# Optimization experiments

Hardware: AMD Instinct MI355X
Metric: run time of the kernel (lower is better)

The kernel has to match this reference:

```python
import jax, jax.numpy as jnp
import numpy as np

NUM_HARMONICS = 64
TEMPERATURE = 1.0

def setup_inputs() -> dict:
    key = jax.random.key(0)
    k1, k2 = jax.random.split(key)
    phases_q = jax.random.normal(k1, (2, 8, 2048, NUM_HARMONICS), dtype=jnp.float32)
    phases_k = jax.random.normal(k2, (2, 8, 2048, NUM_HARMONICS), dtype=jnp.float32)
    return {"phases_q": phases_q, "phases_k": phases_k}

def reference(phases_q, phases_k):
    # mean_h cos(q_h - k_h) = (cos_q @ cos_k^T + sin_q @ sin_k^T) / H
    # (identity: cos(a-b) = cos a cos b + sin a sin b) -- avoids the
    # O(Sq*Sk*H) broadcast intermediate of the naive formulation.
    cq, sq = jnp.cos(phases_q), jnp.sin(phases_q)
    ck, sk = jnp.cos(phases_k), jnp.sin(phases_k)
    coherence = (jnp.einsum('bhqd,bhkd->bhqk', cq, ck) +
                 jnp.einsum('bhqd,bhkd->bhqk', sq, sk)) / NUM_HARMONICS
    return coherence / TEMPERATURE
```

## Files before the change

kernel.cpp:

```cpp
#include <hip/hip_runtime.h>
#include <hip/hip_bf16.h>

#define SEQ 2048
#define NH  64
#define KP  128
#define NBATCH 16
#define STLD 68
#define STSZ (16 * STLD)

typedef __attribute__((ext_vector_type(8))) short  short8;
typedef __attribute__((ext_vector_type(4))) float  floatx4;

static __device__ __forceinline__ unsigned short f2bf(float f) {
    union { float f; unsigned u; } x; x.f = f;
    return (unsigned short)((x.u + 0x7fffu + ((x.u >> 16) & 1u)) >> 16);
}

__global__ void sincos_pack_kernel(const float* __restrict__ pq,
                                   const float* __restrict__ pk,
                                   unsigned short* __restrict__ qpack,
                                   unsigned short* __restrict__ kpack) {
    int i = blockIdx.x * blockDim.x + threadIdx.x;
    const float* src = blockIdx.y ? pk : pq;
    unsigned short* dst = blockIdx.y ? kpack : qpack;
    float4 v = ((const float4*)src)[i];
    int base = i << 2;
    int row  = base >> 6;
    int h    = base & 63;
    float s0, c0, s1, c1, s2, c2, s3, c3;
    __sincosf(v.x, &s0, &c0);
    __sincosf(v.y, &s1, &c1);
    __sincosf(v.z, &s2, &c2);
    __sincosf(v.w, &s3, &c3);
    ushort4 cu; cu.x = f2bf(c0); cu.y = f2bf(c1); cu.z = f2bf(c2); cu.w = f2bf(c3);
    ushort4 su; su.x = f2bf(s0); su.y = f2bf(s1); su.z = f2bf(s2); su.w = f2bf(s3);
    unsigned short* p = dst + (size_t)row * KP + h;
    *(ushort4*)p        = cu;
    *(ushort4*)(p + NH) = su;
}

__global__ __launch_bounds__(256, 2)
void coherence_gemm_kernel(const unsigned short* __restrict__ Qp,
                           const unsigned short* __restrict__ Kp,
                           float* __restrict__ out) {
    __shared__ unsigned short ABs[2 * 128 * KP];
    unsigned short* As = ABs;
    unsigned short* Bs = ABs + 128 * KP;
    const int b  = blockIdx.z;
    const int tm = blockIdx.y;
    const int tn = blockIdx.x;
    const int tid  = threadIdx.x;
    const int wave = tid >> 6;
    const int lane = tid & 63;

    const size_t qbase = (size_t)b * SEQ * KP + (size_t)tm * 128 * KP;
    const size_t kbase = (size_t)b * SEQ * KP + (size_t)tn * 128 * KP;
    const int subrow = lane >> 4;
    const int cslot  = lane & 15;
    for (int it = 0; it < 8; ++it) {
        const int rg = wave * 32 + it * 4;
        const int r  = rg + subrow;
        const int cg = cslot ^ (r & 7);
        const unsigned short* gA = Qp + qbase + (size_t)r * KP + cg * 8;
        const unsigned short* gB = Kp + kbase + (size_t)r * KP + cg * 8;
        unsigned short* lA = As + rg * KP;
        unsigned short* lB = Bs + rg * KP;
        __builtin_amdgcn_global_load_lds(
            (const __attribute__((address_space(1))) void*)gA,
            (__attribute__((address_space(3))) void*)lA, 16, 0, 0);
        __builtin_amdgcn_global_load_lds(
            (const __attribute__((address_space(1))) void*)gB,
            (__attribute__((address_space(3))) void*)lB, 16, 0, 0);
    }
    __syncthreads();

    const int wr = wave >> 1, wc = wave & 1;
    const int qlane = lane >> 4;
    const int mrow  = lane & 15;

    floatx4 acc[4][4] = {};
    #pragma unroll
    for (int ks = 0; ks < 4; ++ks) {
        short8 af[4], bf[4];
        #pragma unroll
        for (int im = 0; im < 4; ++im) {
            const int m = wr * 64 + im * 16 + mrow;
            const int chunk = (ks * 4 + qlane) ^ (m & 7);
            af[im] = *(const short8*)(As + m * KP + chunk * 8);
        }
        #pragma unroll
        for (int in = 0; in < 4; ++in) {
            const int n = wc * 64 + in * 16 + mrow;
            const int chunk = (ks * 4 + qlane) ^ (n & 7);
            bf[in] = *(const short8*)(Bs + n * KP + chunk * 8);
        }
        #pragma unroll
        for (int im = 0; im < 4; ++im)
            #pragma unroll
            for (int in = 0; in < 4; ++in)
                acc[im][in] = __builtin_amdgcn_mfma_f32_16x16x32_bf16(
                    af[im], bf[in], acc[im][in], 0, 0, 0);
    }

    __syncthreads();

    float* st = reinterpret_cast<float*>(ABs) + wave * 2 * STSZ;
    const size_t obase = (size_t)b * SEQ * SEQ + (size_t)(tm * 128) * SEQ + tn * 128;
    const float scale = 1.0f / 64.0f;
    #pragma unroll
    for (int im = 0; im < 4; ++im) {
        float* sb = st + (im & 1) * STSZ;
        #pragma unroll
        for (int in = 0; in < 4; ++in)
            #pragma unroll
            for (int j = 0; j < 4; ++j)
                sb[(qlane * 4 + j) * STLD + in * 16 + mrow] = acc[im][in][j] * scale;
        asm volatile("s_waitcnt lgkmcnt(0)" ::: "memory");
        const size_t rbase = obase + (size_t)(wr * 64 + im * 16) * SEQ
                           + (size_t)(wc * 64 + mrow * 4);
        #pragma unroll
        for (int p = 0; p < 4; ++p) {
            const int rr = p * 4 + qlane;
            const floatx4 v = *(const floatx4*)(sb + rr * STLD + mrow * 4);
            __builtin_nontemporal_store(v, (floatx4*)(out + rbase + (size_t)rr * SEQ));
        }
    }
}

extern "C" void kernel_launch(void* const* d_in, const int* in_sizes, int n_in,
                              void* d_out, int out_size, void* d_ws, size_t ws_size,
                              hipStream_t stream) {
    const float* pq = (const float*)d_in[0];
    const float* pk = (const float*)d_in[1];
    float* out = (float*)d_out;

    unsigned short* qpack = (unsigned short*)d_ws;
    unsigned short* kpack = qpack + (size_t)NBATCH * SEQ * KP;

    const int n4 = NBATCH * SEQ * NH / 4;
    dim3 pgrid(n4 / 256, 2, 1);
    sincos_pack_kernel<<<pgrid, 256, 0, stream>>>(pq, pk, qpack, kpack);

    dim3 ggrid(SEQ / 128, SEQ / 128, NBATCH);
    coherence_gemm_kernel<<<ggrid, 256, 0, stream>>>(qpack, kpack, out);
}
```

Baseline: 287.9 us.

## Fuse sincos/bf16 packing into the GEMM kernel's LDS tile load

After: 307.4 us. 6.8% more time.

```diff
diff --git a/kernel.cpp b/kernel.cpp
--- a/kernel.cpp
+++ b/kernel.cpp
@@ -16,33 +16,10 @@
     return (unsigned short)((x.u + 0x7fffu + ((x.u >> 16) & 1u)) >> 16);
 }
 
-__global__ void sincos_pack_kernel(const float* __restrict__ pq,
-                                   const float* __restrict__ pk,
-                                   unsigned short* __restrict__ qpack,
-                                   unsigned short* __restrict__ kpack) {
-    int i = blockIdx.x * blockDim.x + threadIdx.x;
-    const float* src = blockIdx.y ? pk : pq;
-    unsigned short* dst = blockIdx.y ? kpack : qpack;
-    float4 v = ((const float4*)src)[i];
-    int base = i << 2;
-    int row  = base >> 6;
-    int h    = base & 63;
-    float s0, c0, s1, c1, s2, c2, s3, c3;
-    __sincosf(v.x, &s0, &c0);
-    __sincosf(v.y, &s1, &c1);
-    __sincosf(v.z, &s2, &c2);
-    __sincosf(v.w, &s3, &c3);
-    ushort4 cu; cu.x = f2bf(c0); cu.y = f2bf(c1); cu.z = f2bf(c2); cu.w = f2bf(c3);
-    ushort4 su; su.x = f2bf(s0); su.y = f2bf(s1); su.z = f2bf(s2); su.w = f2bf(s3);
-    unsigned short* p = dst + (size_t)row * KP + h;
-    *(ushort4*)p        = cu;
-    *(ushort4*)(p + NH) = su;
-}
-
 __global__ __launch_bounds__(256, 2)
-void coherence_gemm_kernel(const unsigned short* __restrict__ Qp,
-                           const unsigned short* __restrict__ Kp,
-                           float* __restrict__ out) {
+void coherence_fused_kernel(const float* __restrict__ Pq,
+                            const float* __restrict__ Pk,
+                            float* __restrict__ out) {
     __shared__ unsigned short ABs[2 * 128 * KP];
     unsigned short* As = ABs;
     unsigned short* Bs = ABs + 128 * KP;
@@ -53,24 +30,29 @@
     const int wave = tid >> 6;
     const int lane = tid & 63;
 
-    const size_t qbase = (size_t)b * SEQ * KP + (size_t)tm * 128 * KP;
-    const size_t kbase = (size_t)b * SEQ * KP + (size_t)tn * 128 * KP;
-    const int subrow = lane >> 4;
-    const int cslot  = lane & 15;
-    for (int it = 0; it < 8; ++it) {
-        const int rg = wave * 32 + it * 4;
-        const int r  = rg + subrow;
-        const int cg = cslot ^ (r & 7);
-        const unsigned short* gA = Qp + qbase + (size_t)r * KP + cg * 8;
-        const unsigned short* gB = Kp + kbase + (size_t)r * KP + cg * 8;
-        unsigned short* lA = As + rg * KP;
-        unsigned short* lB = Bs + rg * KP;
-        __builtin_amdgcn_global_load_lds(
-            (const __attribute__((address_space(1))) void*)gA,
-            (__attribute__((address_space(3))) void*)lA, 16, 0, 0);
-        __builtin_amdgcn_global_load_lds(
-            (const __attribute__((address_space(1))) void*)gB,
-            (__attribute__((address_space(3))) void*)lB, 16, 0, 0);
+    {
+        const bool isB = wave >= 2;
+        const int  r   = (wave & 1) * 64 + lane;
+        const float* src = (isB ? Pk : Pq)
+            + ((size_t)b * SEQ + (size_t)(isB ? tn : tm) * 128 + r) * NH;
+        unsigned short* dst = (isB ? Bs : As) + r * KP;
+        const int rs = r & 7;
+        #pragma unroll
+        for (int it = 0; it < 8; ++it) {
+            const float4 va = *(const float4*)(src + it * 8);
+            const float4 vb = *(const float4*)(src + it * 8 + 4);
+            float ph[8] = {va.x, va.y, va.z, va.w, vb.x, vb.y, vb.z, vb.w};
+            short8 cv, sv;
+            #pragma unroll
+            for (int j = 0; j < 8; ++j) {
+                float sn, cs;
+                __sincosf(ph[j], &sn, &cs);
+                cv[j] = (short)f2bf(cs);
+                sv[j] = (short)f2bf(sn);
+            }
+            *(short8*)(dst + ((it ^ rs) * 8))       = cv;
+            *(short8*)(dst + (((8 + it) ^ rs) * 8)) = sv;
+        }
     }
     __syncthreads();
 
@@ -134,13 +116,6 @@
     const float* pk = (const float*)d_in[1];
     float* out = (float*)d_out;
 
-    unsigned short* qpack = (unsigned short*)d_ws;
-    unsigned short* kpack = qpack + (size_t)NBATCH * SEQ * KP;
-
-    const int n4 = NBATCH * SEQ * NH / 4;
-    dim3 pgrid(n4 / 256, 2, 1);
-    sincos_pack_kernel<<<pgrid, 256, 0, stream>>>(pq, pk, qpack, kpack);
-
     dim3 ggrid(SEQ / 128, SEQ / 128, NBATCH);
-    coherence_gemm_kernel<<<ggrid, 256, 0, stream>>>(qpack, kpack, out);
+    coherence_fused_kernel<<<ggrid, 256, 0, stream>>>(pq, pk, out);
 }
```
